# Performance work log

Measured on AMD Instinct MI355X. Metric: run time of the kernel, lower is better.

## Reference

```python
import jax, jax.numpy as jnp
import numpy as np

V, E, H, K, B, T = 50000, 256, 256, 9, 128, 512


def lstm_dir(x, lens, Wih, Whh, b):
    # x: [B,T,E] -> h outputs [B,T,H], packed-sequence semantics:
    # state frozen and outputs zeroed for t >= lens[b].
    Bs, Ts, _ = x.shape
    Hh = Whh.shape[1]
    xw = jnp.einsum('bte,ge->btg', x, Wih) + b  # [B,T,4H] precomputed input proj
    valid = jnp.arange(Ts)[None, :] < lens[:, None]  # [B,T]

    def step(carry, inp):
        h, c = carry
        xw_t, v = inp  # [B,4H], [B]
        gates = xw_t + h @ Whh.T
        i, f, g, o = jnp.split(gates, 4, axis=-1)  # torch gate order i,f,g,o
        i = jax.nn.sigmoid(i)
        f = jax.nn.sigmoid(f)
        g = jnp.tanh(g)
        o = jax.nn.sigmoid(o)
        c_new = f * c + i * g
        h_new = o * jnp.tanh(c_new)
        v = v[:, None]
        return (jnp.where(v, h_new, h), jnp.where(v, c_new, c)), h_new * v

    init = (jnp.zeros((Bs, Hh), x.dtype), jnp.zeros((Bs, Hh), x.dtype))
    _, ys = jax.lax.scan(step, init, (jnp.swapaxes(xw, 0, 1), valid.T))
    return jnp.swapaxes(ys, 0, 1)


def reverse_by_len(x, lens):
    # per-row reversal within valid length; padding stays zero
    Ts = x.shape[1]
    t = jnp.arange(Ts)
    idx = jnp.clip(lens[:, None] - 1 - t[None, :], 0, Ts - 1)
    m = t[None, :] < lens[:, None]
    return jnp.take_along_axis(x, idx[:, :, None], axis=1) * m[:, :, None]


def crf_llh(em, tags, lens, start, end, trans):
    # torchcrf forward with reduction='sum': sum_b (gold score - logZ)
    Bs, Ts, Kk = em.shape
    mask = jnp.arange(Ts)[None, :] < lens[:, None]
    em_t = jnp.take_along_axis(em, tags[..., None], axis=-1)[..., 0]  # [B,T]
    score = start[tags[:, 0]] + em_t[:, 0]
    tr = trans[tags[:, :-1], tags[:, 1:]]  # [B,T-1]
    score = score + jnp.sum((tr + em_t[:, 1:]) * mask[:, 1:], axis=1)
    last_tag = jnp.take_along_axis(tags, (lens - 1)[:, None], axis=1)[:, 0]
    score = score + end[last_tag]

    def step(alpha, inp):
        e_t, m_t = inp  # [B,K], [B]
        nxt = jax.nn.logsumexp(alpha[:, :, None] + trans[None, :, :], axis=1) + e_t
        return jnp.where(m_t[:, None], nxt, alpha), None

    alpha0 = start[None, :] + em[:, 0]  # [B,K]
    alpha, _ = jax.lax.scan(step, alpha0,
                            (jnp.swapaxes(em[:, 1:], 0, 1), mask[:, 1:].T))
    logZ = jax.nn.logsumexp(alpha + end[None, :], axis=1)
    return jnp.sum(score - logZ)


def setup_inputs() -> dict:
    key = jax.random.key(0)
    ks = jax.random.split(key, 16)
    sentences = jax.random.randint(ks[0], (B, T), 0, V)
    tags = jax.random.randint(ks[1], (B, T), 0, K)
    length_list = jax.random.randint(ks[2], (B,), 1, T + 1)  # >=1 so mask[:,0] all true
    s = float(1.0 / np.sqrt(H))
    u = lambda k, sh: jax.random.uniform(k, sh, jnp.float32, -s, s)
    emb = jax.random.normal(ks[3], (V, E), jnp.float32) * float(np.sqrt(2.0 / E))
    return dict(
        sentences=sentences, tags=tags, length_list=length_list,
        emb=emb,
        Wih_f=u(ks[4], (4 * H, E)), Whh_f=u(ks[5], (4 * H, H)), b_f=u(ks[6], (4 * H,)),
        Wih_b=u(ks[7], (4 * H, E)), Whh_b=u(ks[8], (4 * H, H)), b_b=u(ks[9], (4 * H,)),
        W_out=u(ks[10], (K, 2 * H)), b_out=u(ks[11], (K,)),
        start=jax.random.uniform(ks[12], (K,), jnp.float32, -0.1, 0.1),
        end=jax.random.uniform(ks[13], (K,), jnp.float32, -0.1, 0.1),
        trans=jax.random.uniform(ks[14], (K, K), jnp.float32, -0.1, 0.1),
    )


def reference(sentences, tags, length_list, emb, Wih_f, Whh_f, b_f,
              Wih_b, Whh_b, b_b, W_out, b_out, start, end, trans):
    x = emb[sentences]  # [B,T,E]
    h_f = lstm_dir(x, length_list, Wih_f, Whh_f, b_f)
    x_rev = reverse_by_len(x, length_list)
    h_b = reverse_by_len(lstm_dir(x_rev, length_list, Wih_b, Whh_b, b_b), length_list)
    hcat = jnp.concatenate([h_f, h_b], axis=-1)  # [B,T,2H]
    # Dropout is identity in eval mode
    em = jnp.einsum('bth,kh->btk', hcat, W_out) + b_out  # [B,T,K]
    return crf_llh(em, tags, length_list, start, end, trans)
```

## Files before the change

kernel.cpp:

```cpp
#include <hip/hip_runtime.h>
#include <hip/hip_bf16.h>

typedef short v8s __attribute__((ext_vector_type(8)));
typedef int   v8i __attribute__((ext_vector_type(8)));
typedef int   v4i __attribute__((ext_vector_type(4)));
typedef float v4f __attribute__((ext_vector_type(4)));
typedef float v2f __attribute__((ext_vector_type(2)));

#define T_ 512

template<int HI>
__device__ __forceinline__ v2f cvt2(unsigned int wsrc){
  return __builtin_amdgcn_cvt_pk_f32_fp8((int)wsrc, HI);
}
__device__ __forceinline__ v2f rcp2(v2f d){
  return (v2f){__builtin_amdgcn_rcpf(d.x), __builtin_amdgcn_rcpf(d.y)};
}
__device__ __forceinline__ v2f tanh2(v2f x){
  v2f x2 = x*x;
  v2f num = x*(x2 + 27.f);
  v2f den = x2*9.f + 27.f;
  v2f r = num * rcp2(den);
  return (v2f){__builtin_amdgcn_fmed3f(r.x,-1.f,1.f),
               __builtin_amdgcn_fmed3f(r.y,-1.f,1.f)};
}
__device__ __forceinline__ v2f sigm2(v2f x){
  v2f y = x*0.5f;
  v2f y2 = y*y;
  v2f num = y*(y2 + 27.f);
  v2f den = y2*9.f + 27.f;
  v2f r = num * rcp2(den);
  v2f rc = (v2f){__builtin_amdgcn_fmed3f(r.x,-1.f,1.f),
                 __builtin_amdgcn_fmed3f(r.y,-1.f,1.f)};
  return rc*0.5f + 0.5f;
}
__device__ __forceinline__ int pi_col(int p){
  return ((p>>5)<<5) + ((p&1)<<4) + ((p&31)>>1);
}
__device__ __forceinline__ v8i ld32(const void* p){
  uint4 lo = *(const uint4*)p;
  uint4 hi = *(const uint4*)((const char*)p + 16);
  v8i r;
  r[0]=(int)lo.x; r[1]=(int)lo.y; r[2]=(int)lo.z; r[3]=(int)lo.w;
  r[4]=(int)hi.x; r[5]=(int)hi.y; r[6]=(int)hi.z; r[7]=(int)hi.w;
  return r;
}
__device__ __forceinline__ unsigned f2fp4(float x){
  unsigned s = (x < 0.f) ? 8u : 0u;
  float a = fabsf(x);
  unsigned m;
  if      (a < 0.25f) m=0u; else if (a < 0.75f) m=1u;
  else if (a < 1.25f) m=2u; else if (a < 1.75f) m=3u;
  else if (a < 2.5f ) m=4u; else if (a < 3.5f ) m=5u;
  else if (a < 5.f  ) m=6u; else m=7u;
  return s|m;
}
__device__ __forceinline__ unsigned pk8(float a, float b, float c, float d){
  int w = __builtin_amdgcn_cvt_pk_fp8_f32(a, b, 0, 0);
  w     = __builtin_amdgcn_cvt_pk_fp8_f32(c, d, w, 1);
  return (unsigned)w;
}

__global__ __launch_bounds__(256) void prep_wih8_k(
    const float* __restrict__ Wa, const float* __restrict__ Wb,
    unsigned char* __restrict__ out)
{
  int idx = blockIdx.x*256 + threadIdx.x;
  int lane = idx & 63;
  int t2 = idx >> 6;
  int ntile = t2 & 127;
  int kt = t2 >> 7;
  int n = ntile*16 + (lane&15);
  const float* W = (n < 1024) ? (Wa + (size_t)n*256) : (Wb + (size_t)(n-1024)*256);
  int k0 = kt*128 + (lane>>4)*32;
  unsigned words[8];
  #pragma unroll
  for (int e=0;e<8;++e)
    words[e] = pk8(W[k0+e*4], W[k0+e*4+1], W[k0+e*4+2], W[k0+e*4+3]);
  unsigned char* d = out + (size_t)idx*32;
  *(uint4*)(d)      = make_uint4(words[0], words[1], words[2], words[3]);
  *(uint4*)(d + 16) = make_uint4(words[4], words[5], words[6], words[7]);
}

__global__ __launch_bounds__(256) void prep_whh4_k(
    const float* __restrict__ Wf, const float* __restrict__ Wb,
    unsigned char* __restrict__ out)
{
  int idx = blockIdx.x*256 + threadIdx.x;
  int lane = idx & 63;
  int t2 = idx >> 6;
  int ntile = t2 & 63;
  int kt = (t2>>6) & 1;
  int dir = t2 >> 7;
  const float* W = dir ? Wb : Wf;
  int n = ntile*16 + (lane&15);
  int kbase = kt*128 + (lane>>4)*32;
  const float* row = W + (size_t)n*256;
  unsigned words[4];
  #pragma unroll
  for (int d4=0;d4<4;++d4){
    unsigned acc = 0;
    #pragma unroll
    for (int j=0;j<8;++j){
      float v = row[pi_col(kbase + d4*8 + j)] * 64.f;
      acc |= f2fp4(v) << (4*j);
    }
    words[d4] = acc;
  }
  *(uint4*)(out + (size_t)idx*16) = make_uint4(words[0], words[1], words[2], words[3]);
}

__global__ __launch_bounds__(256) void xw_gemm_k(
    const int* __restrict__ sent, const float* __restrict__ emb,
    const unsigned char* __restrict__ wihg, const int* __restrict__ lens,
    const float* __restrict__ bfv, const float* __restrict__ bbv,
    unsigned char* __restrict__ xw)
{
  int mt = blockIdx.x;
  if (((mt&3)<<7) >= lens[mt>>2]) return;
  __shared__ unsigned char A[128][272];
  int tid = threadIdx.x;
  {
    int row = tid>>1, half = tid&1;
    int tok = sent[mt*128 + row];
    const float4* s = (const float4*)(emb + (size_t)tok*256 + half*128);
    unsigned char* drow = &A[row][half*128];
    #pragma unroll
    for (int c4=0; c4<8; ++c4){
      unsigned w0[4];
      #pragma unroll
      for (int u=0; u<4; ++u){
        float4 v = s[c4*4+u];
        w0[u] = pk8(v.x, v.y, v.z, v.w);
      }
      *(uint4*)(drow + c4*16) = make_uint4(w0[0], w0[1], w0[2], w0[3]);
    }
  }
  __syncthreads();
  int w = tid>>6, lane = tid&63, lr = lane&15, lq = lane>>4;
  #pragma unroll 1
  for (int i4=0; i4<4; ++i4){
    int dnv = w*4 + i4;
    int dn = dnv>>3, v = dnv&7;
    const float* bb = dn ? bbv : bfv;
    float bias[8];
    #pragma unroll
    for (int e=0;e<8;++e){
      int q = e>>1, s = e&1;
      bias[e] = bb[q*256 + v*32 + s*16 + lr];
    }
    #pragma unroll 1
    for (int mh=0; mh<2; ++mh){
      v4f acc[8][4];
      #pragma unroll
      for (int e=0;e<8;++e)
        #pragma unroll
        for (int mm=0;mm<4;++mm) acc[e][mm] = (v4f){0.f,0.f,0.f,0.f};
      #pragma unroll
      for (int kt=0;kt<2;++kt){
        v8i a0 = ld32(&A[mh*64 +  0 + lr][kt*128 + lq*32]);
        v8i a1 = ld32(&A[mh*64 + 16 + lr][kt*128 + lq*32]);
        v8i a2 = ld32(&A[mh*64 + 32 + lr][kt*128 + lq*32]);
        v8i a3 = ld32(&A[mh*64 + 48 + lr][kt*128 + lq*32]);
        #pragma unroll
        for (int e=0;e<8;++e){
          int q = e>>1, s = e&1;
          int ntile = dn*64 + q*16 + v*2 + s;
          v8i bfr = ld32(wihg + ((size_t)(kt*128 + ntile)*64 + lane)*32);
          acc[e][0] = __builtin_amdgcn_mfma_scale_f32_16x16x128_f8f6f4(
                        a0, bfr, acc[e][0], 0,0, 0,0x7f7f7f7f, 0,0x7f7f7f7f);
          acc[e][1] = __builtin_amdgcn_mfma_scale_f32_16x16x128_f8f6f4(
                        a1, bfr, acc[e][1], 0,0, 0,0x7f7f7f7f, 0,0x7f7f7f7f);
          acc[e][2] = __builtin_amdgcn_mfma_scale_f32_16x16x128_f8f6f4(
                        a2, bfr, acc[e][2], 0,0, 0,0x7f7f7f7f, 0,0x7f7f7f7f);
          acc[e][3] = __builtin_amdgcn_mfma_scale_f32_16x16x128_f8f6f4(
                        a3, bfr, acc[e][3], 0,0, 0,0x7f7f7f7f, 0,0x7f7f7f7f);
        }
      }
      #pragma unroll
      for (int mm=0;mm<4;++mm){
        #pragma unroll
        for (int j=0;j<4;++j){
          int row = mt*128 + mh*64 + mm*16 + lq*4 + j;
          unsigned lo = pk8(acc[0][mm][j]+bias[0], acc[1][mm][j]+bias[1],
                            acc[2][mm][j]+bias[2], acc[3][mm][j]+bias[3]);
          unsigned hi = pk8(acc[4][mm][j]+bias[4], acc[5][mm][j]+bias[5],
                            acc[6][mm][j]+bias[6], acc[7][mm][j]+bias[7]);
          *(uint2*)(xw + ((size_t)dn*65536 + row)*1024 + v*128 + lr*8)
              = make_uint2(lo, hi);
        }
      }
    }
  }
}

__global__ __launch_bounds__(512,2) void lstm_k(
    const unsigned char* __restrict__ xw,
    const unsigned char* __restrict__ whh4,
    const int* __restrict__ lens,
    unsigned char* __restrict__ hout)
{
  int bid = blockIdx.x, dir = bid>>5, grp = bid&31;
  int tid = threadIdx.x, w = tid>>6, lane = tid&63, lr = lane&15, lq = lane>>4;
  __shared__ unsigned char hbuf[2][16][272];
  __shared__ int tmax_s;
  for (int i=tid*4; i<2*16*272; i+=512*4) *(unsigned int*)(&((unsigned char*)hbuf)[i]) = 0u;
  if (tid==0){
    int mx=0;
    for (int i=0;i<4;++i){ int l = lens[grp*4+i]; mx = l>mx? l:mx; }
    tmax_s = mx;
  }
  v8i wreg[16];
  const unsigned char* wb = whh4 + (size_t)dir*131072;
  #pragma unroll
  for (int kt=0;kt<2;++kt){
    #pragma unroll
    for (int nt=0;nt<8;++nt){
      int ntile = (nt>>1)*16 + w*2 + (nt&1);
      uint4 t = *(const uint4*)(wb + ((size_t)(kt*64 + ntile)*64 + lane)*16);
      v8i r;
      r[0]=(int)t.x; r[1]=(int)t.y; r[2]=(int)t.z; r[3]=(int)t.w;
      r[4]=0; r[5]=0; r[6]=0; r[7]=0;
      wreg[kt*8+nt] = r;
    }
  }
  int seq = grp*4 + lq;
  int ln = lens[seq];
  v2f cc = (v2f){0.f, 0.f};
  const size_t dbase = (size_t)dir*65536;
  const unsigned char* xbase = xw + (dbase + (size_t)seq*T_)*1024 + w*128 + lr*8;
  unsigned char* hbase = hout + (dbase + (size_t)seq*T_)*256 + w*32 + lr*2;
  unsigned char* lw0 = &hbuf[1][lq*4][w*32 + lr*2];
  unsigned char* lw1 = &hbuf[0][lq*4][w*32 + lr*2];
  const unsigned char* lr0 = &hbuf[0][lr][lq*32];
  const unsigned char* lr1 = &hbuf[1][lr][lq*32];
  __syncthreads();
  int tmax = tmax_s;
  uint2 xv = *(const uint2*)(xbase + (size_t)(dir ? (ln-1) : 0)*1024);

  #define STEP_BODY(TE_EXPR, POS_EXPR)                                         \
    int cur = t&1;                                                             \
    int tn = (t+1<tmax)? t+1 : t;                                              \
    int te = (TE_EXPR);                                                        \
    uint2 xn = *(const uint2*)(xbase + ((size_t)te<<10));                      \
    const unsigned char* lrd = cur? lr1 : lr0;                                 \
       \
    v2f xi = cvt2<0>(xv.x), xf = cvt2<1>(xv.x);                                \
    v2f xg = cvt2<0>(xv.y), xo = cvt2<1>(xv.y);                                \
    v4f acc[8];                                                                \
    _Pragma("unroll")                                                          \
    for (int nt=0;nt<8;++nt) asm("" : "=v"(acc[nt]));                          \
    acc[0][0] = xi.x; acc[1][0] = xi.y;                                        \
    acc[2][0] = xf.x; acc[3][0] = xf.y;                                        \
    acc[4][0] = xg.x; acc[5][0] = xg.y;                                        \
    acc[6][0] = xo.x; acc[7][0] = xo.y;                                        \
    _Pragma("unroll")                                                          \
    for (int kt=0;kt<2;++kt){                                                  \
      v8i a = ld32(lrd + kt*128);                                              \
      _Pragma("unroll")                                                        \
      for (int nt=0;nt<8;++nt)                                                 \
        acc[nt] = __builtin_amdgcn_mfma_scale_f32_16x16x128_f8f6f4(            \
                    a, wreg[kt*8+nt], acc[nt], 0, 4, 0, 0x7f7f7f7f, 0, 0x79797979); \
    }                                                                          \
    bool valid = t < ln;                                                       \
    int pos = (POS_EXPR);                                                      \
    v2f gi = (v2f){acc[0][0], acc[1][0]};                                      \
    v2f gf = (v2f){acc[2][0], acc[3][0]};                                      \
    v2f gg = (v2f){acc[4][0], acc[5][0]};                                      \
    v2f go = (v2f){acc[6][0], acc[7][0]};                                      \
    v2f iv = sigm2(gi), fv = sigm2(gf), gv = tanh2(gg), ov = sigm2(go);        \
    v2f cn = fv*cc + iv*gv;                                                    \
    v2f hn = ov*tanh2(cn);                                                     \
    int hp = __builtin_amdgcn_cvt_pk_fp8_f32(hn.x, hn.y, 0, 0);                \
    unsigned short hu = valid ? (unsigned short)(hp & 0xffff) : (unsigned short)0; \
    if (valid){                                                                \
      cc = cn;                                                                 \
      *(unsigned short*)(cur? lw1 : lw0) = hu;                                 \
    }                                                                          \
    *(unsigned short*)(hbase + ((size_t)pos<<8)) = hu;                         \
    xv = xn;                                                                   \
    asm volatile("s_waitcnt lgkmcnt(0)" ::: "memory");                         \
    __builtin_amdgcn_s_barrier();                                              \
    __builtin_amdgcn_sched_barrier(0);

  if (dir == 0){
    for (int t=0; t<tmax; ++t){
      STEP_BODY(tn, t)
    }
  } else {
    for (int t=0; t<tmax; ++t){
      STEP_BODY((tn<ln)? (ln-1-tn) : tn, valid? (ln-1-t) : t)
    }
  }
  #undef STEP_BODY
}

__global__ __launch_bounds__(256) void em_k(
    const unsigned char* __restrict__ hout,
    const float* __restrict__ Wout, const float* __restrict__ bout,
    const int* __restrict__ lens,
    float* __restrict__ em)
{
  __shared__ float Ws[9*512];
  for (int i=threadIdx.x;i<9*512;i+=256){
    int k = i>>9, p = i&511;
    int d = p>>8, pp = p&255;
    Ws[i] = Wout[k*512 + d*256 + pi_col(pp)];
  }
  __syncthreads();
  int wv = blockIdx.x*4 + (threadIdx.x>>6);
  int lane = threadIdx.x & 63;
  int g = lane>>4, r = lane&15;
  int m = wv*4 + g;
  const unsigned char* hf = hout + (size_t)m*256 + r*16;
  const unsigned char* hb = hout + ((size_t)65536 + m)*256 + r*16;
  uint4 vf = *(const uint4*)hf;
  uint4 vb = *(const uint4*)hb;
  float xf[16], xb[16];
  {
    v2f d0=cvt2<0>(vf.x), d1=cvt2<1>(vf.x), d2=cvt2<0>(vf.y), d3=cvt2<1>(vf.y);
    v2f d4=cvt2<0>(vf.z), d5=cvt2<1>(vf.z), d6=cvt2<0>(vf.w), d7=cvt2<1>(vf.w);
    xf[0]=d0.x; xf[1]=d0.y; xf[2]=d1.x; xf[3]=d1.y;
    xf[4]=d2.x; xf[5]=d2.y; xf[6]=d3.x; xf[7]=d3.y;
    xf[8]=d4.x; xf[9]=d4.y; xf[10]=d5.x; xf[11]=d5.y;
    xf[12]=d6.x; xf[13]=d6.y; xf[14]=d7.x; xf[15]=d7.y;
  }
  {
    v2f d0=cvt2<0>(vb.x), d1=cvt2<1>(vb.x), d2=cvt2<0>(vb.y), d3=cvt2<1>(vb.y);
    v2f d4=cvt2<0>(vb.z), d5=cvt2<1>(vb.z), d6=cvt2<0>(vb.w), d7=cvt2<1>(vb.w);
    xb[0]=d0.x; xb[1]=d0.y; xb[2]=d1.x; xb[3]=d1.y;
    xb[4]=d2.x; xb[5]=d2.y; xb[6]=d3.x; xb[7]=d3.y;
    xb[8]=d4.x; xb[9]=d4.y; xb[10]=d5.x; xb[11]=d5.y;
    xb[12]=d6.x; xb[13]=d6.y; xb[14]=d7.x; xb[15]=d7.y;
  }
  float a[9];
  #pragma unroll
  for (int k=0;k<9;++k){
    float s = 0.f;
    #pragma unroll
    for (int e=0;e<16;++e)
      s += xf[e]*Ws[k*512 + r*16 + e] + xb[e]*Ws[k*512 + 256 + r*16 + e];
    a[k]=s;
  }
  #pragma unroll
  for (int k=0;k<9;++k){
    #pragma unroll
    for (int off=8; off; off>>=1) a[k] += __shfl_xor(a[k], off, 64);
  }
  int b = m>>9, t = m&511;
  if (r==0 && t < lens[b]){
    float* d = em + (size_t)m*9;
    #pragma unroll
    for (int k=0;k<9;++k) d[k] = a[k] + bout[k];
  }
}

__global__ __launch_bounds__(256) void crf_k(
    const float* __restrict__ em, const int* __restrict__ tags,
    const int* __restrict__ lens, const float* __restrict__ startv,
    const float* __restrict__ endv, const float* __restrict__ trans,
    float* __restrict__ out)
{
  int wid = blockIdx.x*4 + (threadIdx.x>>6);
  int lane = threadIdx.x & 63;
  const float* e = em + (size_t)wid*T_*9;
  const int* tg = tags + (size_t)wid*T_;
  int L = lens[wid];
  float p = 0.f;
  for (int t = 1+lane; t < L; t += 64)
    p += trans[tg[t-1]*9 + tg[t]] + e[(size_t)t*9 + tg[t]];
  if (lane==0) p += startv[tg[0]] + e[tg[0]] + endv[tg[L-1]];
  #pragma unroll
  for (int off=32; off; off>>=1) p += __shfl_xor(p, off, 64);
  float tcol[9];
  #pragma unroll
  for (int i=0;i<9;++i) tcol[i] = (lane<9) ? trans[i*9 + lane] : 0.f;
  float alpha = (lane<9) ? (startv[lane] + e[lane]) : -1e30f;
  for (int t=1; t<L; ++t){
    float vs[9]; float mx = -1e30f;
    #pragma unroll
    for (int i=0;i<9;++i){
      float ai = __shfl(alpha, i, 64);
      vs[i] = ai + tcol[i];
      mx = fmaxf(mx, vs[i]);
    }
    float s = 0.f;
    #pragma unroll
    for (int i=0;i<9;++i) s += __expf(vs[i]-mx);
    float na = mx + __logf(s) + ((lane<9)? e[(size_t)t*9+lane] : 0.f);
    alpha = (lane<9) ? na : -1e30f;
  }
  float v = (lane<9) ? (alpha + endv[lane]) : -1e30f;
  float mx = v;
  #pragma unroll
  for (int off=32; off; off>>=1) mx = fmaxf(mx, __shfl_xor(mx, off, 64));
  float s = __expf(v-mx);
  #pragma unroll
  for (int off=32; off; off>>=1) s += __shfl_xor(s, off, 64);
  float logZ = mx + __logf(s);
  if (lane==0) atomicAdd(out, p - logZ);
}

extern "C" void kernel_launch(void* const* d_in, const int* in_sizes, int n_in,
                              void* d_out, int out_size, void* d_ws, size_t ws_size,
                              hipStream_t stream)
{
  const int*   sent  = (const int*)d_in[0];
  const int*   tags  = (const int*)d_in[1];
  const int*   lens  = (const int*)d_in[2];
  const float* emb   = (const float*)d_in[3];
  const float* Wih_f = (const float*)d_in[4];
  const float* Whh_f = (const float*)d_in[5];
  const float* b_f   = (const float*)d_in[6];
  const float* Wih_b = (const float*)d_in[7];
  const float* Whh_b = (const float*)d_in[8];
  const float* b_b   = (const float*)d_in[9];
  const float* Wout  = (const float*)d_in[10];
  const float* bout  = (const float*)d_in[11];
  const float* startv= (const float*)d_in[12];
  const float* endv  = (const float*)d_in[13];
  const float* trans = (const float*)d_in[14];
  char* ws = (char*)d_ws;
  unsigned char* wihg8 = (unsigned char*)(ws);
  unsigned char* whh4  = (unsigned char*)(ws + (size_t)524288);
  unsigned char* xw    = (unsigned char*)(ws + (size_t)1048576);
  unsigned char* hout  = (unsigned char*)(ws + (size_t)135266304);
  float* em            = (float*)(ws + (size_t)168820736);
  float* outp = (float*)d_out;

  (void)hipMemsetAsync(outp, 0, sizeof(float), stream);
  prep_wih8_k<<<64, 256, 0, stream>>>(Wih_f, Wih_b, wihg8);
  prep_whh4_k<<<64, 256, 0, stream>>>(Whh_f, Whh_b, whh4);
  xw_gemm_k<<<512, 256, 0, stream>>>(sent, emb, wihg8, lens, b_f, b_b, xw);
  lstm_k<<<64, 512, 0, stream>>>(xw, whh4, lens, hout);
  em_k<<<4096, 256, 0, stream>>>(hout, Wout, bout, lens, em);
  crf_k<<<32, 256, 0, stream>>>(em, tags, lens, startv, endv, trans, outp);
}
```

Before: 705.1 us.

## Interleave forward and backward LSTM directions within one block

Each LSTM block now runs both the forward and the backward direction for its group of 4 sequences, holding both recurrent weight sets in registers. The launch drops from 64 to 32 blocks. Two independent recurrences share each step's barrier, so the MFMA and activation work of one direction can hide the latency of the other and the per-step synchronisation cost is amortised. In exchange each block needs twice the weight registers, which may cause spills or lower occupancy, and fewer blocks are active on the device.

Result: slower. 1.134 ms (+60.8%).

```diff
diff --git a/kernel.cpp b/kernel.cpp
--- a/kernel.cpp
+++ b/kernel.cpp
@@ -200,99 +200,114 @@
     const int* __restrict__ lens,
     unsigned char* __restrict__ hout)
 {
-  int bid = blockIdx.x, dir = bid>>5, grp = bid&31;
+  int grp = blockIdx.x;
   int tid = threadIdx.x, w = tid>>6, lane = tid&63, lr = lane&15, lq = lane>>4;
-  __shared__ unsigned char hbuf[2][16][272];
+  __shared__ unsigned char hb[2][2][16][272];
   __shared__ int tmax_s;
-  for (int i=tid*4; i<2*16*272; i+=512*4) *(unsigned int*)(&((unsigned char*)hbuf)[i]) = 0u;
+  for (int i=tid*4; i<2*2*16*272; i+=512*4) *(unsigned int*)(&((unsigned char*)hb)[i]) = 0u;
   if (tid==0){
     int mx=0;
     for (int i=0;i<4;++i){ int l = lens[grp*4+i]; mx = l>mx? l:mx; }
     tmax_s = mx;
   }
-  v8i wreg[16];
-  const unsigned char* wb = whh4 + (size_t)dir*131072;
+  v8i wregA[16], wregB[16];
   #pragma unroll
   for (int kt=0;kt<2;++kt){
     #pragma unroll
     for (int nt=0;nt<8;++nt){
       int ntile = (nt>>1)*16 + w*2 + (nt&1);
-      uint4 t = *(const uint4*)(wb + ((size_t)(kt*64 + ntile)*64 + lane)*16);
-      v8i r;
-      r[0]=(int)t.x; r[1]=(int)t.y; r[2]=(int)t.z; r[3]=(int)t.w;
-      r[4]=0; r[5]=0; r[6]=0; r[7]=0;
-      wreg[kt*8+nt] = r;
+      size_t off = ((size_t)(kt*64 + ntile)*64 + lane)*16;
+      uint4 ta = *(const uint4*)(whh4 + off);
+      uint4 tb = *(const uint4*)(whh4 + 131072 + off);
+      v8i ra; ra[0]=(int)ta.x; ra[1]=(int)ta.y; ra[2]=(int)ta.z; ra[3]=(int)ta.w;
+      ra[4]=0; ra[5]=0; ra[6]=0; ra[7]=0;
+      v8i rb; rb[0]=(int)tb.x; rb[1]=(int)tb.y; rb[2]=(int)tb.z; rb[3]=(int)tb.w;
+      rb[4]=0; rb[5]=0; rb[6]=0; rb[7]=0;
+      wregA[kt*8+nt] = ra;
+      wregB[kt*8+nt] = rb;
     }
   }
   int seq = grp*4 + lq;
   int ln = lens[seq];
-  v2f cc = (v2f){0.f, 0.f};
-  const size_t dbase = (size_t)dir*65536;
-  const unsigned char* xbase = xw + (dbase + (size_t)seq*T_)*1024 + w*128 + lr*8;
-  unsigned char* hbase = hout + (dbase + (size_t)seq*T_)*256 + w*32 + lr*2;
-  unsigned char* lw0 = &hbuf[1][lq*4][w*32 + lr*2];
-  unsigned char* lw1 = &hbuf[0][lq*4][w*32 + lr*2];
-  const unsigned char* lr0 = &hbuf[0][lr][lq*32];
-  const unsigned char* lr1 = &hbuf[1][lr][lq*32];
+  v2f cc0 = (v2f){0.f,0.f}, cc1 = (v2f){0.f,0.f};
+  const unsigned char* xb0 = xw + ((size_t)seq*T_)*1024 + w*128 + lr*8;
+  const unsigned char* xb1 = xw + ((size_t)65536 + (size_t)seq*T_)*1024 + w*128 + lr*8;
+  unsigned char* ho0 = hout + ((size_t)seq*T_)*256 + w*32 + lr*2;
+  unsigned char* ho1 = hout + ((size_t)65536 + (size_t)seq*T_)*256 + w*32 + lr*2;
+  const unsigned char* rA0 = &hb[0][0][lr][lq*32];
+  const unsigned char* rA1 = &hb[1][0][lr][lq*32];
+  const unsigned char* rB0 = &hb[0][1][lr][lq*32];
+  const unsigned char* rB1 = &hb[1][1][lr][lq*32];
+  unsigned char* wA0 = &hb[1][0][lq*4][w*32 + lr*2];
+  unsigned char* wA1 = &hb[0][0][lq*4][w*32 + lr*2];
+  unsigned char* wB0 = &hb[1][1][lq*4][w*32 + lr*2];
+  unsigned char* wB1 = &hb[0][1][lq*4][w*32 + lr*2];
   __syncthreads();
   int tmax = tmax_s;
-  uint2 xv = *(const uint2*)(xbase + (size_t)(dir ? (ln-1) : 0)*1024);
-
-  #define STEP_BODY(TE_EXPR, POS_EXPR)                                         \
-    int cur = t&1;                                                             \
-    int tn = (t+1<tmax)? t+1 : t;                                              \
-    int te = (TE_EXPR);                                                        \
-    uint2 xn = *(const uint2*)(xbase + ((size_t)te<<10));                      \
-    const unsigned char* lrd = cur? lr1 : lr0;                                 \
-       \
-    v2f xi = cvt2<0>(xv.x), xf = cvt2<1>(xv.x);                                \
-    v2f xg = cvt2<0>(xv.y), xo = cvt2<1>(xv.y);                                \
-    v4f acc[8];                                                                \
-    _Pragma("unroll")                                                          \
-    for (int nt=0;nt<8;++nt) asm("" : "=v"(acc[nt]));                          \
-    acc[0][0] = xi.x; acc[1][0] = xi.y;                                        \
-    acc[2][0] = xf.x; acc[3][0] = xf.y;                                        \
-    acc[4][0] = xg.x; acc[5][0] = xg.y;                                        \
-    acc[6][0] = xo.x; acc[7][0] = xo.y;                                        \
-    _Pragma("unroll")                                                          \
-    for (int kt=0;kt<2;++kt){                                                  \
-      v8i a = ld32(lrd + kt*128);                                              \
-      _Pragma("unroll")                                                        \
-      for (int nt=0;nt<8;++nt)                                                 \
-        acc[nt] = __builtin_amdgcn_mfma_scale_f32_16x16x128_f8f6f4(            \
-                    a, wreg[kt*8+nt], acc[nt], 0, 4, 0, 0x7f7f7f7f, 0, 0x79797979); \
-    }                                                                          \
-    bool valid = t < ln;                                                       \
-    int pos = (POS_EXPR);                                                      \
-    v2f gi = (v2f){acc[0][0], acc[1][0]};                                      \
-    v2f gf = (v2f){acc[2][0], acc[3][0]};                                      \
-    v2f gg = (v2f){acc[4][0], acc[5][0]};                                      \
-    v2f go = (v2f){acc[6][0], acc[7][0]};                                      \
-    v2f iv = sigm2(gi), fv = sigm2(gf), gv = tanh2(gg), ov = sigm2(go);        \
-    v2f cn = fv*cc + iv*gv;                                                    \
-    v2f hn = ov*tanh2(cn);                                                     \
-    int hp = __builtin_amdgcn_cvt_pk_fp8_f32(hn.x, hn.y, 0, 0);                \
-    unsigned short hu = valid ? (unsigned short)(hp & 0xffff) : (unsigned short)0; \
-    if (valid){                                                                \
-      cc = cn;                                                                 \
-      *(unsigned short*)(cur? lw1 : lw0) = hu;                                 \
-    }                                                                          \
-    *(unsigned short*)(hbase + ((size_t)pos<<8)) = hu;                         \
-    xv = xn;                                                                   \
-    asm volatile("s_waitcnt lgkmcnt(0)" ::: "memory");                         \
-    __builtin_amdgcn_s_barrier();                                              \
+  uint2 xv0 = *(const uint2*)(xb0);
+  uint2 xv1 = *(const uint2*)(xb1 + ((size_t)(ln-1)<<10));
+  for (int t=0; t<tmax; ++t){
+    int cur = t&1;
+    int tn = (t+1<tmax)? t+1 : t;
+    int te1 = (tn<ln)? (ln-1-tn) : tn;
+    uint2 xn0 = *(const uint2*)(xb0 + ((size_t)tn<<10));
+    uint2 xn1 = *(const uint2*)(xb1 + ((size_t)te1<<10));
+    const unsigned char* r0 = cur? rA1 : rA0;
+    const unsigned char* r1 = cur? rB1 : rB0;
+    v2f xi0=cvt2<0>(xv0.x), xf0=cvt2<1>(xv0.x), xg0=cvt2<0>(xv0.y), xo0=cvt2<1>(xv0.y);
+    v2f xi1=cvt2<0>(xv1.x), xf1=cvt2<1>(xv1.x), xg1=cvt2<0>(xv1.y), xo1=cvt2<1>(xv1.y);
+    v4f a0[8], a1[8];
+    #pragma unroll
+    for (int nt=0;nt<8;++nt){ asm("" : "=v"(a0[nt])); asm("" : "=v"(a1[nt])); }
+    a0[0][0]=xi0.x; a0[1][0]=xi0.y; a0[2][0]=xf0.x; a0[3][0]=xf0.y;
+    a0[4][0]=xg0.x; a0[5][0]=xg0.y; a0[6][0]=xo0.x; a0[7][0]=xo0.y;
+    a1[0][0]=xi1.x; a1[1][0]=xi1.y; a1[2][0]=xf1.x; a1[3][0]=xf1.y;
+    a1[4][0]=xg1.x; a1[5][0]=xg1.y; a1[6][0]=xo1.x; a1[7][0]=xo1.y;
+    #pragma unroll
+    for (int kt=0;kt<2;++kt){
+      v8i av = ld32(r0 + kt*128);
+      #pragma unroll
+      for (int nt=0;nt<8;++nt)
+        a0[nt] = __builtin_amdgcn_mfma_scale_f32_16x16x128_f8f6f4(
+                   av, wregA[kt*8+nt], a0[nt], 0, 4, 0, 0x7f7f7f7f, 0, 0x79797979);
+    }
+    #pragma unroll
+    for (int kt=0;kt<2;++kt){
+      v8i av = ld32(r1 + kt*128);
+      #pragma unroll
+      for (int nt=0;nt<8;++nt)
+        a1[nt] = __builtin_amdgcn_mfma_scale_f32_16x16x128_f8f6f4(
+                   av, wregB[kt*8+nt], a1[nt], 0, 4, 0, 0x7f7f7f7f, 0, 0x79797979);
+    }
+    bool valid = t < ln;
+    int pos1 = valid? (ln-1-t) : t;
+    {
+      v2f gi=(v2f){a0[0][0],a0[1][0]}, gf=(v2f){a0[2][0],a0[3][0]};
+      v2f gg=(v2f){a0[4][0],a0[5][0]}, go=(v2f){a0[6][0],a0[7][0]};
+      v2f iv=sigm2(gi), fv=sigm2(gf), gv=tanh2(gg), ov=sigm2(go);
+      v2f cn = fv*cc0 + iv*gv;
+      v2f hn = ov*tanh2(cn);
+      int hp = __builtin_amdgcn_cvt_pk_fp8_f32(hn.x, hn.y, 0, 0);
+      unsigned short hu = valid ? (unsigned short)(hp & 0xffff) : (unsigned short)0;
+      if (valid){ cc0 = cn; *(unsigned short*)(cur? wA1 : wA0) = hu; }
+      *(unsigned short*)(ho0 + ((size_t)t<<8)) = hu;
+    }
+    {
+      v2f gi=(v2f){a1[0][0],a1[1][0]}, gf=(v2f){a1[2][0],a1[3][0]};
+      v2f gg=(v2f){a1[4][0],a1[5][0]}, go=(v2f){a1[6][0],a1[7][0]};
+      v2f iv=sigm2(gi), fv=sigm2(gf), gv=tanh2(gg), ov=sigm2(go);
+      v2f cn = fv*cc1 + iv*gv;
+      v2f hn = ov*tanh2(cn);
+      int hp = __builtin_amdgcn_cvt_pk_fp8_f32(hn.x, hn.y, 0, 0);
+      unsigned short hu = valid ? (unsigned short)(hp & 0xffff) : (unsigned short)0;
+      if (valid){ cc1 = cn; *(unsigned short*)(cur? wB1 : wB0) = hu; }
+      *(unsigned short*)(ho1 + ((size_t)pos1<<8)) = hu;
+    }
+    xv0 = xn0; xv1 = xn1;
+    asm volatile("s_waitcnt lgkmcnt(0)" ::: "memory");
+    __builtin_amdgcn_s_barrier();
     __builtin_amdgcn_sched_barrier(0);
-
-  if (dir == 0){
-    for (int t=0; t<tmax; ++t){
-      STEP_BODY(tn, t)
-    }
-  } else {
-    for (int t=0; t<tmax; ++t){
-      STEP_BODY((tn<ln)? (ln-1-tn) : tn, valid? (ln-1-t) : t)
-    }
-  }
-  #undef STEP_BODY
+  }
 }
 
 __global__ __launch_bounds__(256) void em_k(
@@ -432,7 +447,7 @@
   prep_wih8_k<<<64, 256, 0, stream>>>(Wih_f, Wih_b, wihg8);
   prep_whh4_k<<<64, 256, 0, stream>>>(Whh_f, Whh_b, whh4);
   xw_gemm_k<<<512, 256, 0, stream>>>(sent, emb, wihg8, lens, b_f, b_b, xw);
-  lstm_k<<<64, 512, 0, stream>>>(xw, whh4, lens, hout);
+  lstm_k<<<32, 512, 0, stream>>>(xw, whh4, lens, hout);
   em_k<<<4096, 256, 0, stream>>>(hout, Wout, bout, lens, em);
   crf_k<<<32, 256, 0, stream>>>(em, tags, lens, startv, endv, trans, outp);
 }
```

## Quantize recurrent hidden state to FP4 for MFMA and drop validity masking

Applied to the files above, without the earlier changes.

Stores the recurrent hidden state in shared memory as FP4 instead of FP8, using a custom enc4 encoder. The MFMA A operand switches to the fp4 format with an adjusted scale, which halves the LDS footprint and the per-step read size. It also removes the per-step validity branch, so the cell state and shared buffer update unconditionally. It relies on later stages masking outputs past the sequence length, and it changes launch bounds to one block per SIMD. FP4 hidden state is a large precision loss on the recurrence and risks accuracy drift over 512 steps, and the extra encode ALU work sits on the serial critical path.

Result: no change. 704.5 us (-0.1%).

```diff
diff --git a/kernel.cpp b/kernel.cpp
--- a/kernel.cpp
+++ b/kernel.cpp
@@ -3,7 +3,6 @@
 
 typedef short v8s __attribute__((ext_vector_type(8)));
 typedef int   v8i __attribute__((ext_vector_type(8)));
-typedef int   v4i __attribute__((ext_vector_type(4)));
 typedef float v4f __attribute__((ext_vector_type(4)));
 typedef float v2f __attribute__((ext_vector_type(2)));
 
@@ -59,6 +58,23 @@
   int w = __builtin_amdgcn_cvt_pk_fp8_f32(a, b, 0, 0);
   w     = __builtin_amdgcn_cvt_pk_fp8_f32(c, d, w, 1);
   return (unsigned)w;
+}
+__device__ __forceinline__ unsigned enc4(v2f h){
+  v2f t = h*4.f;
+  unsigned b = 0;
+  #pragma unroll
+  for (int s=0;s<2;++s){
+    float v = s ? t.y : t.x;
+    float ax = __builtin_amdgcn_fmed3f(fabsf(v), 0.f, 4.f);
+    float gl = fmaf(ax, 2.f, 12582912.f);
+    float gh = ax + 12582912.f;
+    unsigned ql = __builtin_bit_cast(unsigned, gl) & 7u;
+    unsigned qh = (__builtin_bit_cast(unsigned, gh) & 7u) + 2u;
+    unsigned c  = (ax > 1.75f) ? qh : ql;
+    unsigned sg = (__builtin_bit_cast(unsigned, v) >> 28) & 8u;
+    b |= (c | sg) << (4*s);
+  }
+  return b;
 }
 
 __global__ __launch_bounds__(256) void prep_wih8_k(
@@ -194,7 +210,7 @@
   }
 }
 
-__global__ __launch_bounds__(512,2) void lstm_k(
+__global__ __launch_bounds__(512,1) void lstm_k(
     const unsigned char* __restrict__ xw,
     const unsigned char* __restrict__ whh4,
     const int* __restrict__ lens,
@@ -202,9 +218,9 @@
 {
   int bid = blockIdx.x, dir = bid>>5, grp = bid&31;
   int tid = threadIdx.x, w = tid>>6, lane = tid&63, lr = lane&15, lq = lane>>4;
-  __shared__ unsigned char hbuf[2][16][272];
+  __shared__ unsigned char hbuf[2][16][136];
   __shared__ int tmax_s;
-  for (int i=tid*4; i<2*16*272; i+=512*4) *(unsigned int*)(&((unsigned char*)hbuf)[i]) = 0u;
+  for (int i=tid*4; i<2*16*136; i+=512*4) *(unsigned int*)(&((unsigned char*)hbuf)[i]) = 0u;
   if (tid==0){
     int mx=0;
     for (int i=0;i<4;++i){ int l = lens[grp*4+i]; mx = l>mx? l:mx; }
@@ -230,10 +246,10 @@
   const size_t dbase = (size_t)dir*65536;
   const unsigned char* xbase = xw + (dbase + (size_t)seq*T_)*1024 + w*128 + lr*8;
   unsigned char* hbase = hout + (dbase + (size_t)seq*T_)*256 + w*32 + lr*2;
-  unsigned char* lw0 = &hbuf[1][lq*4][w*32 + lr*2];
-  unsigned char* lw1 = &hbuf[0][lq*4][w*32 + lr*2];
-  const unsigned char* lr0 = &hbuf[0][lr][lq*32];
-  const unsigned char* lr1 = &hbuf[1][lr][lq*32];
+  unsigned char* lw0 = &hbuf[1][lq*4][w*16 + lr];
+  unsigned char* lw1 = &hbuf[0][lq*4][w*16 + lr];
+  const unsigned char* lr0 = &hbuf[0][lr][lq*16];
+  const unsigned char* lr1 = &hbuf[1][lr][lq*16];
   __syncthreads();
   int tmax = tmax_s;
   uint2 xv = *(const uint2*)(xbase + (size_t)(dir ? (ln-1) : 0)*1024);
@@ -244,7 +260,6 @@
     int te = (TE_EXPR);                                                        \
     uint2 xn = *(const uint2*)(xbase + ((size_t)te<<10));                      \
     const unsigned char* lrd = cur? lr1 : lr0;                                 \
-       \
     v2f xi = cvt2<0>(xv.x), xf = cvt2<1>(xv.x);                                \
     v2f xg = cvt2<0>(xv.y), xo = cvt2<1>(xv.y);                                \
     v4f acc[8];                                                                \
@@ -256,13 +271,16 @@
     acc[6][0] = xo.x; acc[7][0] = xo.y;                                        \
     _Pragma("unroll")                                                          \
     for (int kt=0;kt<2;++kt){                                                  \
-      v8i a = ld32(lrd + kt*128);                                              \
+      uint4 hh = *(const uint4*)(lrd + kt*64);                                 \
+      v8i a;                                                                   \
+      a[0]=(int)hh.x; a[1]=(int)hh.y; a[2]=(int)hh.z; a[3]=(int)hh.w;          \
+      a[4]=0; a[5]=0; a[6]=0; a[7]=0;                                          \
       _Pragma("unroll")                                                        \
       for (int nt=0;nt<8;++nt)                                                 \
         acc[nt] = __builtin_amdgcn_mfma_scale_f32_16x16x128_f8f6f4(            \
-                    a, wreg[kt*8+nt], acc[nt], 0, 4, 0, 0x7f7f7f7f, 0, 0x79797979); \
+                    a, wreg[kt*8+nt], acc[nt], 4, 4,                           \
+                    0, 0x7D7D7D7D, 0, 0x79797979);                             \
     }                                                                          \
-    bool valid = t < ln;                                                       \
     int pos = (POS_EXPR);                                                      \
     v2f gi = (v2f){acc[0][0], acc[1][0]};                                      \
     v2f gf = (v2f){acc[2][0], acc[3][0]};                                      \
@@ -271,13 +289,10 @@
     v2f iv = sigm2(gi), fv = sigm2(gf), gv = tanh2(gg), ov = sigm2(go);        \
     v2f cn = fv*cc + iv*gv;                                                    \
     v2f hn = ov*tanh2(cn);                                                     \
+    cc = cn;                                                                   \
     int hp = __builtin_amdgcn_cvt_pk_fp8_f32(hn.x, hn.y, 0, 0);                \
-    unsigned short hu = valid ? (unsigned short)(hp & 0xffff) : (unsigned short)0; \
-    if (valid){                                                                \
-      cc = cn;                                                                 \
-      *(unsigned short*)(cur? lw1 : lw0) = hu;                                 \
-    }                                                                          \
-    *(unsigned short*)(hbase + ((size_t)pos<<8)) = hu;                         \
+    *(unsigned short*)(hbase + ((size_t)pos<<8)) = (unsigned short)(hp&0xffff);\
+    *(cur? lw1 : lw0) = (unsigned char)enc4(hn);                               \
     xv = xn;                                                                   \
     asm volatile("s_waitcnt lgkmcnt(0)" ::: "memory");                         \
     __builtin_amdgcn_s_barrier();                                              \
@@ -289,7 +304,7 @@
     }
   } else {
     for (int t=0; t<tmax; ++t){
-      STEP_BODY((tn<ln)? (ln-1-tn) : tn, valid? (ln-1-t) : t)
+      STEP_BODY((tn<ln)? (ln-1-tn) : tn, (t<ln)? (ln-1-t) : t)
     }
   }
   #undef STEP_BODY
```
